# Optimization experiments

Hardware: AMD Instinct MI355X
Metric: run time of the kernel (lower is better)

The kernel has to match this reference:

```python
import jax, jax.numpy as jnp
import numpy as np

E = 8          # num_experts
TOP_K = 2
CAP_RATIO = 1.2


def setup_inputs() -> dict:
    key = jax.random.key(0)
    k1, k2, k3, k4 = jax.random.split(key, 4)
    B, L, D, H = 2, 2048, 768, 2048
    x = jax.random.normal(k1, (B, L, D), dtype=jnp.float32)
    Wg = jax.random.normal(k2, (D, E), dtype=jnp.float32) * 0.02   # gate: Linear(D, E, bias=False)
    W1 = jax.random.normal(k3, (E, D, 2 * H), dtype=jnp.float32) * 0.02  # fc1 per expert (y | gate halves)
    W2 = jax.random.normal(k4, (E, H, D), dtype=jnp.float32) * 0.02      # fc2 per expert
    return {"x": x, "Wg": Wg, "W1": W1, "W2": W2}


def reference(x, Wg, W1, W2):
    B, L, D = x.shape
    H = W2.shape[1]
    xf = x.reshape(-1, D)                      # [N, D]
    N = xf.shape[0]
    capacity = int(CAP_RATIO * N / E)          # static, matches torch int()

    logits = xf @ Wg                           # [N, E]
    scores, idx = jax.lax.top_k(logits, TOP_K) # [N, K] (descending, like torch.topk)
    weights = jax.nn.softmax(scores, axis=-1)  # [N, K]

    # padded token table: row N is a zero token used for unfilled capacity slots
    xpad = jnp.concatenate([xf, jnp.zeros((1, D), xf.dtype)], axis=0)
    wpad_zero = jnp.zeros((1,), weights.dtype)
    out = jnp.zeros((N, D), x.dtype)

    for k in range(TOP_K):
        ik = idx[:, k]                                         # [N] expert id per token
        onehot = (ik[:, None] == jnp.arange(E)[None, :])       # [N, E]
        pos = jnp.cumsum(onehot, axis=0) - 1                   # rank within expert, ascending token order
        posk = jnp.take_along_axis(pos, ik[:, None], axis=1)[:, 0]  # [N]
        keep = posk < capacity                                 # first-come capacity (== indices[:capacity])

        # dispatch buffer [E, C]: token index per slot, N (pad) where unfilled/dropped
        buf = jnp.full((E, capacity), N, dtype=jnp.int32)
        buf = buf.at[ik, posk].set(jnp.arange(N, dtype=jnp.int32), mode="drop")

        xg = xpad[buf]                                         # [E, C, D]
        h = jnp.einsum("ecd,edh->ech", xg, W1)                 # [E, C, 2H]
        act = h[..., :H] * jax.nn.silu(h[..., H:])             # GatedMLP: y * silu(gate)
        ye = jnp.einsum("ech,ehd->ecd", act, W2)               # [E, C, D]

        wk = jnp.where(keep, weights[:, k], 0.0)               # [N]
        w_buf = jnp.concatenate([wk, wpad_zero])[buf]          # [E, C], 0 on pad slots
        out = out.at[buf.reshape(-1)].add(
            (w_buf[..., None] * ye).reshape(E * capacity, D), mode="drop"
        )

    return out.reshape(B, L, D)
```

## Files before the change

### kernel.cpp

```cpp
#include <hip/hip_runtime.h>


typedef _Float16 half8 __attribute__((ext_vector_type(8)));
typedef _Float16 half4t __attribute__((ext_vector_type(4)));
typedef float f4 __attribute__((ext_vector_type(4)));

#define N_TOK 4096
#define DDIM  768
#define HDIM  2048
#define NEXP  8
#define CAP   614
#define CAPP  640

#define XH_OFF    0L
#define W1T_OFF   6292992L
#define W2T_OFF   56624640L
#define ACT_OFF   81790464L
#define EIDX_OFF  123733504L
#define WTS_OFF   123766272L
#define TOKL_OFF  123799040L
#define CNT_OFF   123840000L

__device__ __forceinline__ void gld16(const void* g, void* l) {
  __builtin_amdgcn_global_load_lds(
      (const __attribute__((address_space(1))) unsigned int*)g,
      (__attribute__((address_space(3))) unsigned int*)l, 16, 0, 0);
}

__global__ __launch_bounds__(256) void cvt_tr_kernel(const float* __restrict__ src,
                                                     _Float16* __restrict__ dst,
                                                     int R, int C) {
  __shared__ float tile[64 * 69];
  int e = blockIdx.z;
  int r0 = blockIdx.x * 64, c0 = blockIdx.y * 64;
  long sb = (long)e * R * C;
  int t = threadIdx.x;
  int rrow = t >> 4, c4 = (t & 15) * 4;
#pragma unroll
  for (int i = 0; i < 4; i++) {
    int row = i * 16 + rrow;
    f4 v = *(const f4*)(src + sb + (long)(r0 + row) * C + c0 + c4);
    *(f4*)(&tile[row * 69 + c4]) = v;
  }
  __syncthreads();
#pragma unroll
  for (int s = 0; s < 2; s++) {
    int idx = t + s * 256;
    int c = idx >> 3, ch = idx & 7;
    half8 h;
#pragma unroll
    for (int j = 0; j < 8; j++) h[j] = (_Float16)tile[(ch * 8 + j) * 69 + c];
    *(half8*)(dst + sb + (long)(c0 + c) * R + r0 + ch * 8) = h;
  }
}

__global__ __launch_bounds__(256) void router_kernel(const float* __restrict__ x,
                                                     const float* __restrict__ Wg,
                                                     _Float16* __restrict__ xh,
                                                     int* __restrict__ eidx,
                                                     float* __restrict__ wts) {
  __shared__ float wgT[NEXP * DDIM];
  int t = threadIdx.x;
  for (int i = t; i < DDIM * NEXP; i += 256) wgT[(i & 7) * DDIM + (i >> 3)] = Wg[i];
  __syncthreads();
  int w = t >> 6, lane = t & 63;
  int tok = blockIdx.x * 4 + w;
  if (tok > N_TOK) return;
  if (tok == N_TOK) {
    half4t zz; zz[0] = zz[1] = zz[2] = zz[3] = (_Float16)0.f;
#pragma unroll
    for (int j = 0; j < 3; j++) *(half4t*)(xh + (long)N_TOK * DDIM + (lane + j * 64) * 4) = zz;
    return;
  }
  const float* xr = x + (long)tok * DDIM;
#pragma unroll
  for (int j = 0; j < 3; j++) {
    f4 v = *(const f4*)(xr + (lane + j * 64) * 4);
    half4t hv;
    hv[0] = (_Float16)v[0]; hv[1] = (_Float16)v[1];
    hv[2] = (_Float16)v[2]; hv[3] = (_Float16)v[3];
    *(half4t*)(xh + (long)tok * DDIM + (lane + j * 64) * 4) = hv;
  }
  float acc[8] = {0.f, 0.f, 0.f, 0.f, 0.f, 0.f, 0.f, 0.f};
#pragma unroll
  for (int i = 0; i < 12; i++) {
    float xv = xr[i * 64 + lane];
#pragma unroll
    for (int e2 = 0; e2 < 8; e2++) acc[e2] += xv * wgT[e2 * DDIM + i * 64 + lane];
  }
#pragma unroll
  for (int e2 = 0; e2 < 8; e2++) {
    float v = acc[e2];
    v += __shfl_xor(v, 32); v += __shfl_xor(v, 16); v += __shfl_xor(v, 8);
    v += __shfl_xor(v, 4);  v += __shfl_xor(v, 2);  v += __shfl_xor(v, 1);
    acc[e2] = v;
  }
  if (lane == 0) {
    float m0 = -1e30f; int i0 = 0;
#pragma unroll
    for (int e2 = 0; e2 < 8; e2++) if (acc[e2] > m0) { m0 = acc[e2]; i0 = e2; }
    float m1 = -1e30f; int i1 = 0;
#pragma unroll
    for (int e2 = 0; e2 < 8; e2++) if (e2 != i0 && acc[e2] > m1) { m1 = acc[e2]; i1 = e2; }
    float tt = __expf(m1 - m0);
    float w0 = 1.f / (1.f + tt);
    eidx[tok * 2 + 0] = i0; eidx[tok * 2 + 1] = i1;
    wts[tok * 2 + 0] = w0;  wts[tok * 2 + 1] = 1.f - w0;
  }
}

__global__ __launch_bounds__(64) void scan_kernel(const int* __restrict__ eidx,
                                                  int* __restrict__ toklist,
                                                  int* __restrict__ counts) {
  int z = blockIdx.x;
  int k = z >> 3, e = z & 7;
  int lane = threadIdx.x;
  int mye[64];
#pragma unroll
  for (int c = 0; c < 64; c++) mye[c] = eidx[(c * 64 + lane) * 2 + k];
  int base = 0;
#pragma unroll 4
  for (int c = 0; c < 64; c++) {
    int n = c * 64 + lane;
    bool pred = (mye[c] == e);
    unsigned long long mask = __ballot(pred);
    if (pred) {
      int pos = base + __popcll(mask & ((1ull << lane) - 1ull));
      if (pos < CAP) toklist[z * CAPP + pos] = n;
    }
    base += __popcll(mask);
  }
  if (lane == 0) counts[z] = (base < CAP) ? base : CAP;
}

__global__ __launch_bounds__(512, 2) void gemm1_kernel(const _Float16* __restrict__ xh,
                                                       const _Float16* __restrict__ w1t,
                                                       const int* __restrict__ toklist,
                                                       const int* __restrict__ counts,
                                                       _Float16* __restrict__ act) {
  int i = blockIdx.x;
  int e = i & 7, j = i >> 3;
  int m = j % 3, nk = j / 3;
  int k = nk & 1, n = nk >> 1;
  int z = k * 8 + e;
  int count = counts[z];
  int m0 = m * 256;
  if (m0 >= count) return;
  int n0 = n * 128;

  __shared__ _Float16 lds[2][32768];

  int t = threadIdx.x;
  int u = t & 7, rg = t >> 3;
  int swz = (u ^ (rg & 7)) * 8;

  int tokr[4];
#pragma unroll
  for (int s = 0; s < 4; s++) {
    int r = m0 + s * 64 + rg;
    tokr[s] = (r < count) ? toklist[z * CAPP + r] : N_TOK;
  }

  const _Float16* ag[4];
  const _Float16* bg[4];
  int adst[4], bdst[4];
#pragma unroll
  for (int s = 0; s < 4; s++) {
    int row = s * 64 + rg;
    ag[s] = xh + (long)tokr[s] * DDIM + swz;
    adst[s] = row * 64 + u * 8;
    int rb = row;
    int hc = n0 + ((rb >> 6) << 5) + (rb & 31) + ((rb >> 5) & 1) * 2048;
    bg[s] = w1t + ((long)e * 4096 + hc) * DDIM + swz;
    bdst[s] = 16384 + rb * 64 + u * 8;
  }

  int lane = t & 63, wid = t >> 6;
  int wm = wid >> 2, wn = wid & 3;
  int q = lane >> 4, m16 = lane & 15;

  f4 zero4 = {0.f, 0.f, 0.f, 0.f};
  f4 acc[8][4];
#pragma unroll
  for (int mt = 0; mt < 8; mt++)
#pragma unroll
    for (int ct = 0; ct < 4; ct++) acc[mt][ct] = zero4;

  asm volatile("s_waitcnt vmcnt(0)" ::: "memory");
  __builtin_amdgcn_sched_barrier(0);

#pragma unroll
  for (int s = 0; s < 4; s++) gld16(ag[s], &lds[0][adst[s]]);
#pragma unroll
  for (int s = 0; s < 4; s++) gld16(bg[s], &lds[0][bdst[s]]);
#pragma unroll
  for (int s = 0; s < 4; s++) gld16(ag[s] + 64, &lds[1][adst[s]]);
#pragma unroll
  for (int s = 0; s < 4; s++) gld16(bg[s] + 64, &lds[1][bdst[s]]);
#pragma unroll
  for (int s = 0; s < 4; s++) { ag[s] += 128; bg[s] += 128; }

  for (int t2 = 0; t2 < 12; t2++) {
    int p = t2 & 1;
    const _Float16* A = &lds[p][0];
    const _Float16* B = &lds[p][16384];
    if (t2 < 11) { asm volatile("s_waitcnt vmcnt(8)" ::: "memory"); }
    else         { asm volatile("s_waitcnt vmcnt(0)" ::: "memory"); }
    __builtin_amdgcn_sched_barrier(0);
    __builtin_amdgcn_s_barrier();
    __builtin_amdgcn_sched_barrier(0);

#pragma unroll
    for (int kk = 0; kk < 2; kk++) {
      half8 bfr[4];
#pragma unroll
      for (int ct = 0; ct < 4; ct++) {
        int rb = wn * 64 + ct * 16 + m16;
        bfr[ct] = *(const half8*)(B + rb * 64 + (((kk * 4 + q) ^ (rb & 7)) * 8));
      }
      __builtin_amdgcn_s_setprio(1);
#pragma unroll
      for (int mt = 0; mt < 8; mt++) {
        int row = wm * 128 + mt * 16 + m16;
        half8 a = *(const half8*)(A + row * 64 + (((kk * 4 + q) ^ (row & 7)) * 8));
#pragma unroll
        for (int ct = 0; ct < 4; ct++)
          acc[mt][ct] = __builtin_amdgcn_mfma_f32_16x16x32_f16(a, bfr[ct], acc[mt][ct], 0, 0, 0);
      }
      __builtin_amdgcn_s_setprio(0);
    }
    asm volatile("s_waitcnt lgkmcnt(0)" ::: "memory");
    __builtin_amdgcn_sched_barrier(0);
    __builtin_amdgcn_s_barrier();
    __builtin_amdgcn_sched_barrier(0);
    if (t2 < 10) {
#pragma unroll
      for (int s = 0; s < 4; s++) gld16(ag[s], &lds[p][adst[s]]);
#pragma unroll
      for (int s = 0; s < 4; s++) gld16(bg[s], &lds[p][bdst[s]]);
#pragma unroll
      for (int s = 0; s < 4; s++) { ag[s] += 64; bg[s] += 64; }
    }
    __builtin_amdgcn_sched_barrier(0);
  }

  long ab = (long)z * CAPP * HDIM;
#pragma unroll
  for (int mt = 0; mt < 8; mt++) {
    int row0 = m0 + wm * 128 + mt * 16 + q * 4;
#pragma unroll
    for (int cp = 0; cp < 2; cp++) {
      int col = n0 + wn * 32 + cp * 16 + m16;
#pragma unroll
      for (int r = 0; r < 4; r++) {
        int row = row0 + r;
        if (row < CAPP) {
          float h1 = acc[mt][cp][r], h2 = acc[mt][2 + cp][r];
          float s = h2 / (1.f + __expf(-h2));
          act[ab + (long)row * HDIM + col] = (_Float16)(h1 * s);
        }
      }
    }
  }
}

__global__ __launch_bounds__(512, 2) void gemm2_kernel(const _Float16* __restrict__ act,
                                                       const _Float16* __restrict__ w2t,
                                                       const int* __restrict__ toklist,
                                                       const int* __restrict__ counts,
                                                       const float* __restrict__ wts,
                                                       float* __restrict__ out) {
  int i = blockIdx.x;
  int e = i & 7, j = i >> 3;
  int m = j % 5, nk = j / 5;
  int k = nk & 1, n = nk >> 1;
  int z = k * 8 + e;
  int count = counts[z];
  int m0 = m * 128;
  if (m0 >= count) return;
  int n0 = n * 256;

  __shared__ _Float16 lds[2][24576];
  __shared__ int toksL[128];
  __shared__ float wrow[128];

  int t = threadIdx.x;
  if (t < 128) {
    int r = m0 + t;
    if (r < count) {
      int tok = toklist[z * CAPP + r];
      toksL[t] = tok;
      wrow[t] = wts[tok * 2 + k];
    } else {
      toksL[t] = -1;
      wrow[t] = 0.f;
    }
  }
  __syncthreads();

  int u = t & 7, rg = t >> 3;
  int swz = (u ^ (rg & 7)) * 8;

  const _Float16* ag[2];
  const _Float16* bg[4];
  int adst[2], bdst[4];
#pragma unroll
  for (int s = 0; s < 2; s++) {
    int row = s * 64 + rg;
    ag[s] = act + ((long)z * CAPP + m0 + row) * HDIM + swz;
    adst[s] = row * 64 + u * 8;
  }
#pragma unroll
  for (int s = 0; s < 4; s++) {
    int rb = s * 64 + rg;
    bg[s] = w2t + ((long)e * DDIM + n0 + rb) * HDIM + swz;
    bdst[s] = 8192 + rb * 64 + u * 8;
  }

  int lane = t & 63, wid = t >> 6;
  int wm = wid >> 2, wn = wid & 3;
  int q = lane >> 4, m16 = lane & 15;

  f4 zero4 = {0.f, 0.f, 0.f, 0.f};
  f4 acc[4][4];
#pragma unroll
  for (int mt = 0; mt < 4; mt++)
#pragma unroll
    for (int ct = 0; ct < 4; ct++) acc[mt][ct] = zero4;

#pragma unroll
  for (int s = 0; s < 2; s++) gld16(ag[s], &lds[0][adst[s]]);
#pragma unroll
  for (int s = 0; s < 4; s++) gld16(bg[s], &lds[0][bdst[s]]);
#pragma unroll
  for (int s = 0; s < 2; s++) gld16(ag[s] + 64, &lds[1][adst[s]]);
#pragma unroll
  for (int s = 0; s < 4; s++) gld16(bg[s] + 64, &lds[1][bdst[s]]);
#pragma unroll
  for (int s = 0; s < 2; s++) ag[s] += 128;
#pragma unroll
  for (int s = 0; s < 4; s++) bg[s] += 128;

  for (int t2 = 0; t2 < 32; t2++) {
    int p = t2 & 1;
    const _Float16* A = &lds[p][0];
    const _Float16* B = &lds[p][8192];
    if (t2 < 31) { asm volatile("s_waitcnt vmcnt(6)" ::: "memory"); }
    else         { asm volatile("s_waitcnt vmcnt(0)" ::: "memory"); }
    __builtin_amdgcn_sched_barrier(0);
    __builtin_amdgcn_s_barrier();
    __builtin_amdgcn_sched_barrier(0);

#pragma unroll
    for (int kk = 0; kk < 2; kk++) {
      half8 bfr[4];
#pragma unroll
      for (int ct = 0; ct < 4; ct++) {
        int rb = wn * 64 + ct * 16 + m16;
        bfr[ct] = *(const half8*)(B + rb * 64 + (((kk * 4 + q) ^ (rb & 7)) * 8));
      }
      __builtin_amdgcn_s_setprio(1);
#pragma unroll
      for (int mt = 0; mt < 4; mt++) {
        int row = wm * 64 + mt * 16 + m16;
        half8 a = *(const half8*)(A + row * 64 + (((kk * 4 + q) ^ (row & 7)) * 8));
#pragma unroll
        for (int ct = 0; ct < 4; ct++)
          acc[mt][ct] = __builtin_amdgcn_mfma_f32_16x16x32_f16(a, bfr[ct], acc[mt][ct], 0, 0, 0);
      }
      __builtin_amdgcn_s_setprio(0);
    }
    asm volatile("s_waitcnt lgkmcnt(0)" ::: "memory");
    __builtin_amdgcn_sched_barrier(0);
    __builtin_amdgcn_s_barrier();
    __builtin_amdgcn_sched_barrier(0);
    if (t2 < 30) {
#pragma unroll
      for (int s = 0; s < 2; s++) gld16(ag[s], &lds[p][adst[s]]);
#pragma unroll
      for (int s = 0; s < 4; s++) gld16(bg[s], &lds[p][bdst[s]]);
#pragma unroll
      for (int s = 0; s < 2; s++) ag[s] += 64;
#pragma unroll
      for (int s = 0; s < 4; s++) bg[s] += 64;
    }
    __builtin_amdgcn_sched_barrier(0);
  }

#pragma unroll
  for (int mt = 0; mt < 4; mt++)
#pragma unroll
    for (int ct = 0; ct < 4; ct++)
#pragma unroll
      for (int r = 0; r < 4; r++) {
        int lr = wm * 64 + mt * 16 + q * 4 + r;
        int tok = toksL[lr];
        if (tok >= 0) {
          int col = n0 + wn * 64 + ct * 16 + m16;
          atomicAdd(&out[(long)tok * DDIM + col], wrow[lr] * acc[mt][ct][r]);
        }
      }
}


extern "C" void kernel_launch(void* const* d_in, const int* in_sizes, int n_in,
                              void* d_out, int out_size, void* d_ws, size_t ws_size,
                              hipStream_t stream) {
  const float* x  = (const float*)d_in[0];
  const float* Wg = (const float*)d_in[1];
  const float* W1 = (const float*)d_in[2];
  const float* W2 = (const float*)d_in[3];
  float* out = (float*)d_out;
  char* ws = (char*)d_ws;

  _Float16* xh   = (_Float16*)(ws + XH_OFF);
  _Float16* w1t  = (_Float16*)(ws + W1T_OFF);
  _Float16* w2t  = (_Float16*)(ws + W2T_OFF);
  _Float16* actb = (_Float16*)(ws + ACT_OFF);
  int* eidx      = (int*)(ws + EIDX_OFF);
  float* wts     = (float*)(ws + WTS_OFF);
  int* toklist   = (int*)(ws + TOKL_OFF);
  int* counts    = (int*)(ws + CNT_OFF);

  hipMemsetAsync(d_out, 0, (size_t)out_size * sizeof(float), stream);
  cvt_tr_kernel<<<dim3(12, 64, 8), 256, 0, stream>>>(W1, w1t, 768, 4096);
  cvt_tr_kernel<<<dim3(32, 12, 8), 256, 0, stream>>>(W2, w2t, 2048, 768);
  router_kernel<<<1025, 256, 0, stream>>>(x, Wg, xh, eidx, wts);
  scan_kernel<<<16, 64, 0, stream>>>(eidx, toklist, counts);
  gemm1_kernel<<<768, 512, 0, stream>>>(xh, w1t, toklist, counts, actb);
  gemm2_kernel<<<240, 512, 0, stream>>>(actb, w2t, toklist, counts, wts, out);
}
```

Measured before the change: 369.3 us.

## Triple-buffer LDS in both expert GEMMs and shrink gemm1 M tile to 128

Both grouped GEMM kernels move from a double-buffered to a three-stage rotating LDS ring. Each K-step is split into two half-steps, and the global-to-LDS loads for the stage two ahead are spread across those halves to overlap memory latency with MFMA work. gemm1 also drops its M tile from 256 to 128 rows, raising its grid from 768 to 1280 blocks and halving accumulator registers. In exchange there are more barriers per iteration, more LDS per block (144 KB), and more B-tile reloads for gemm1. The row<CAPP guard in the gemm1 epilogue is removed, which is safe with 128-row tiles because the last tile ends exactly at 640.

```diff
diff --git a/kernel.cpp b/kernel.cpp
--- a/kernel.cpp
+++ b/kernel.cpp
@@ -20,6 +20,8 @@
 #define WTS_OFF   123766272L
 #define TOKL_OFF  123799040L
 #define CNT_OFF   123840000L
+
+#define BUFH 24576
 
 __device__ __forceinline__ void gld16(const void* g, void* l) {
   __builtin_amdgcn_global_load_lds(
@@ -140,39 +142,41 @@
                                                        _Float16* __restrict__ act) {
   int i = blockIdx.x;
   int e = i & 7, j = i >> 3;
-  int m = j % 3, nk = j / 3;
+  int m = j % 5, nk = j / 5;
   int k = nk & 1, n = nk >> 1;
   int z = k * 8 + e;
   int count = counts[z];
-  int m0 = m * 256;
+  int m0 = m * 128;
   if (m0 >= count) return;
   int n0 = n * 128;
 
-  __shared__ _Float16 lds[2][32768];
+  __shared__ _Float16 lds[3 * BUFH];
 
   int t = threadIdx.x;
   int u = t & 7, rg = t >> 3;
   int swz = (u ^ (rg & 7)) * 8;
 
-  int tokr[4];
-#pragma unroll
-  for (int s = 0; s < 4; s++) {
+  int tokr[2];
+#pragma unroll
+  for (int s = 0; s < 2; s++) {
     int r = m0 + s * 64 + rg;
     tokr[s] = (r < count) ? toklist[z * CAPP + r] : N_TOK;
   }
 
-  const _Float16* ag[4];
-  const _Float16* bg[4];
-  int adst[4], bdst[4];
-#pragma unroll
-  for (int s = 0; s < 4; s++) {
+  const _Float16* ag[2]; int adst[2];
+#pragma unroll
+  for (int s = 0; s < 2; s++) {
     int row = s * 64 + rg;
     ag[s] = xh + (long)tokr[s] * DDIM + swz;
     adst[s] = row * 64 + u * 8;
-    int rb = row;
+  }
+  const _Float16* bg[4]; int bdst[4];
+#pragma unroll
+  for (int s = 0; s < 4; s++) {
+    int rb = s * 64 + rg;
     int hc = n0 + ((rb >> 6) << 5) + (rb & 31) + ((rb >> 5) & 1) * 2048;
     bg[s] = w1t + ((long)e * 4096 + hc) * DDIM + swz;
-    bdst[s] = 16384 + rb * 64 + u * 8;
+    bdst[s] = 8192 + rb * 64 + u * 8;
   }
 
   int lane = t & 63, wid = t >> 6;
@@ -180,9 +184,9 @@
   int q = lane >> 4, m16 = lane & 15;
 
   f4 zero4 = {0.f, 0.f, 0.f, 0.f};
-  f4 acc[8][4];
-#pragma unroll
-  for (int mt = 0; mt < 8; mt++)
+  f4 acc[4][4];
+#pragma unroll
+  for (int mt = 0; mt < 4; mt++)
 #pragma unroll
     for (int ct = 0; ct < 4; ct++) acc[mt][ct] = zero4;
 
@@ -190,75 +194,119 @@
   __builtin_amdgcn_sched_barrier(0);
 
 #pragma unroll
-  for (int s = 0; s < 4; s++) gld16(ag[s], &lds[0][adst[s]]);
-#pragma unroll
-  for (int s = 0; s < 4; s++) gld16(bg[s], &lds[0][bdst[s]]);
-#pragma unroll
-  for (int s = 0; s < 4; s++) gld16(ag[s] + 64, &lds[1][adst[s]]);
-#pragma unroll
-  for (int s = 0; s < 4; s++) gld16(bg[s] + 64, &lds[1][bdst[s]]);
-#pragma unroll
-  for (int s = 0; s < 4; s++) { ag[s] += 128; bg[s] += 128; }
+  for (int s = 0; s < 2; s++) gld16(ag[s], &lds[adst[s]]);
+#pragma unroll
+  for (int s = 0; s < 4; s++) gld16(bg[s], &lds[bdst[s]]);
+#pragma unroll
+  for (int s = 0; s < 2; s++) gld16(ag[s] + 64, &lds[BUFH + adst[s]]);
+#pragma unroll
+  for (int s = 0; s < 4; s++) gld16(bg[s] + 64, &lds[BUFH + bdst[s]]);
+#pragma unroll
+  for (int s = 0; s < 2; s++) ag[s] += 128;
+#pragma unroll
+  for (int s = 0; s < 4; s++) bg[s] += 128;
+  asm volatile("s_waitcnt vmcnt(6)" ::: "memory");
+  __builtin_amdgcn_sched_barrier(0);
+  __builtin_amdgcn_s_barrier();
+  __builtin_amdgcn_sched_barrier(0);
+
+  int offR = 0, offM = BUFH, offW = 2 * BUFH;
 
   for (int t2 = 0; t2 < 12; t2++) {
-    int p = t2 & 1;
-    const _Float16* A = &lds[p][0];
-    const _Float16* B = &lds[p][16384];
-    if (t2 < 11) { asm volatile("s_waitcnt vmcnt(8)" ::: "memory"); }
-    else         { asm volatile("s_waitcnt vmcnt(0)" ::: "memory"); }
+    const _Float16* A = &lds[offR];
+    const _Float16* B = &lds[offR + 8192];
+    bool st = (t2 < 10);
+
+    half8 bfr[4][2], afr[2][2];
+#pragma unroll
+    for (int ct = 0; ct < 4; ct++) {
+      int rb = wn * 64 + ct * 16 + m16;
+      bfr[ct][0] = *(const half8*)(B + rb * 64 + (((0 * 4 + q) ^ (rb & 7)) * 8));
+      bfr[ct][1] = *(const half8*)(B + rb * 64 + (((1 * 4 + q) ^ (rb & 7)) * 8));
+    }
+#pragma unroll
+    for (int mt = 0; mt < 2; mt++) {
+      int row = wm * 64 + mt * 16 + m16;
+      afr[mt][0] = *(const half8*)(A + row * 64 + (((0 * 4 + q) ^ (row & 7)) * 8));
+      afr[mt][1] = *(const half8*)(A + row * 64 + (((1 * 4 + q) ^ (row & 7)) * 8));
+    }
+    if (st) {
+      gld16(ag[0], &lds[offW + adst[0]]);
+      gld16(ag[1], &lds[offW + adst[1]]);
+      gld16(bg[0], &lds[offW + bdst[0]]);
+    }
     __builtin_amdgcn_sched_barrier(0);
     __builtin_amdgcn_s_barrier();
     __builtin_amdgcn_sched_barrier(0);
-
-#pragma unroll
-    for (int kk = 0; kk < 2; kk++) {
-      half8 bfr[4];
+    asm volatile("s_waitcnt lgkmcnt(0)" ::: "memory");
+    __builtin_amdgcn_sched_barrier(0);
+    __builtin_amdgcn_s_setprio(1);
+#pragma unroll
+    for (int mt = 0; mt < 2; mt++)
 #pragma unroll
       for (int ct = 0; ct < 4; ct++) {
-        int rb = wn * 64 + ct * 16 + m16;
-        bfr[ct] = *(const half8*)(B + rb * 64 + (((kk * 4 + q) ^ (rb & 7)) * 8));
+        acc[mt][ct] = __builtin_amdgcn_mfma_f32_16x16x32_f16(afr[mt][0], bfr[ct][0], acc[mt][ct], 0, 0, 0);
+        acc[mt][ct] = __builtin_amdgcn_mfma_f32_16x16x32_f16(afr[mt][1], bfr[ct][1], acc[mt][ct], 0, 0, 0);
       }
-      __builtin_amdgcn_s_setprio(1);
-#pragma unroll
-      for (int mt = 0; mt < 8; mt++) {
-        int row = wm * 128 + mt * 16 + m16;
-        half8 a = *(const half8*)(A + row * 64 + (((kk * 4 + q) ^ (row & 7)) * 8));
-#pragma unroll
-        for (int ct = 0; ct < 4; ct++)
-          acc[mt][ct] = __builtin_amdgcn_mfma_f32_16x16x32_f16(a, bfr[ct], acc[mt][ct], 0, 0, 0);
+    __builtin_amdgcn_s_setprio(0);
+    __builtin_amdgcn_sched_barrier(0);
+    __builtin_amdgcn_s_barrier();
+    __builtin_amdgcn_sched_barrier(0);
+
+    half8 afr2[2][2];
+#pragma unroll
+    for (int mt = 0; mt < 2; mt++) {
+      int row = wm * 64 + (2 + mt) * 16 + m16;
+      afr2[mt][0] = *(const half8*)(A + row * 64 + (((0 * 4 + q) ^ (row & 7)) * 8));
+      afr2[mt][1] = *(const half8*)(A + row * 64 + (((1 * 4 + q) ^ (row & 7)) * 8));
+    }
+    if (st) {
+      gld16(bg[1], &lds[offW + bdst[1]]);
+      gld16(bg[2], &lds[offW + bdst[2]]);
+      gld16(bg[3], &lds[offW + bdst[3]]);
+#pragma unroll
+      for (int s = 0; s < 2; s++) ag[s] += 64;
+#pragma unroll
+      for (int s = 0; s < 4; s++) bg[s] += 64;
+    }
+    __builtin_amdgcn_sched_barrier(0);
+    __builtin_amdgcn_s_barrier();
+    __builtin_amdgcn_sched_barrier(0);
+    asm volatile("s_waitcnt lgkmcnt(0)" ::: "memory");
+    __builtin_amdgcn_sched_barrier(0);
+    __builtin_amdgcn_s_setprio(1);
+#pragma unroll
+    for (int mt = 0; mt < 2; mt++)
+#pragma unroll
+      for (int ct = 0; ct < 4; ct++) {
+        acc[2 + mt][ct] = __builtin_amdgcn_mfma_f32_16x16x32_f16(afr2[mt][0], bfr[ct][0], acc[2 + mt][ct], 0, 0, 0);
+        acc[2 + mt][ct] = __builtin_amdgcn_mfma_f32_16x16x32_f16(afr2[mt][1], bfr[ct][1], acc[2 + mt][ct], 0, 0, 0);
       }
-      __builtin_amdgcn_s_setprio(0);
-    }
-    asm volatile("s_waitcnt lgkmcnt(0)" ::: "memory");
-    __builtin_amdgcn_sched_barrier(0);
-    __builtin_amdgcn_s_barrier();
-    __builtin_amdgcn_sched_barrier(0);
-    if (t2 < 10) {
-#pragma unroll
-      for (int s = 0; s < 4; s++) gld16(ag[s], &lds[p][adst[s]]);
-#pragma unroll
-      for (int s = 0; s < 4; s++) gld16(bg[s], &lds[p][bdst[s]]);
-#pragma unroll
-      for (int s = 0; s < 4; s++) { ag[s] += 64; bg[s] += 64; }
-    }
-    __builtin_amdgcn_sched_barrier(0);
+    __builtin_amdgcn_s_setprio(0);
+    __builtin_amdgcn_sched_barrier(0);
+    if (t2 < 10)      { asm volatile("s_waitcnt vmcnt(6)" ::: "memory"); }
+    else if (t2 == 10){ asm volatile("s_waitcnt vmcnt(0)" ::: "memory"); }
+    if (t2 < 11) {
+      __builtin_amdgcn_sched_barrier(0);
+      __builtin_amdgcn_s_barrier();
+      __builtin_amdgcn_sched_barrier(0);
+    }
+    int tmp = offR; offR = offM; offM = offW; offW = tmp;
   }
 
   long ab = (long)z * CAPP * HDIM;
 #pragma unroll
-  for (int mt = 0; mt < 8; mt++) {
-    int row0 = m0 + wm * 128 + mt * 16 + q * 4;
+  for (int mt = 0; mt < 4; mt++) {
+    int row0 = m0 + wm * 64 + mt * 16 + q * 4;
 #pragma unroll
     for (int cp = 0; cp < 2; cp++) {
       int col = n0 + wn * 32 + cp * 16 + m16;
 #pragma unroll
       for (int r = 0; r < 4; r++) {
         int row = row0 + r;
-        if (row < CAPP) {
-          float h1 = acc[mt][cp][r], h2 = acc[mt][2 + cp][r];
-          float s = h2 / (1.f + __expf(-h2));
-          act[ab + (long)row * HDIM + col] = (_Float16)(h1 * s);
-        }
+        float h1 = acc[mt][cp][r], h2 = acc[mt][2 + cp][r];
+        float s = h2 / (1.f + __expf(-h2));
+        act[ab + (long)row * HDIM + col] = (_Float16)(h1 * s);
       }
     }
   }
@@ -280,7 +328,7 @@
   if (m0 >= count) return;
   int n0 = n * 256;
 
-  __shared__ _Float16 lds[2][24576];
+  __shared__ _Float16 lds[3 * BUFH];
   __shared__ int toksL[128];
   __shared__ float wrow[128];
 
@@ -301,15 +349,14 @@
   int u = t & 7, rg = t >> 3;
   int swz = (u ^ (rg & 7)) * 8;
 
-  const _Float16* ag[2];
-  const _Float16* bg[4];
-  int adst[2], bdst[4];
+  const _Float16* ag[2]; int adst[2];
 #pragma unroll
   for (int s = 0; s < 2; s++) {
     int row = s * 64 + rg;
     ag[s] = act + ((long)z * CAPP + m0 + row) * HDIM + swz;
     adst[s] = row * 64 + u * 8;
   }
+  const _Float16* bg[4]; int bdst[4];
 #pragma unroll
   for (int s = 0; s < 4; s++) {
     int rb = s * 64 + rg;
@@ -329,62 +376,104 @@
     for (int ct = 0; ct < 4; ct++) acc[mt][ct] = zero4;
 
 #pragma unroll
-  for (int s = 0; s < 2; s++) gld16(ag[s], &lds[0][adst[s]]);
-#pragma unroll
-  for (int s = 0; s < 4; s++) gld16(bg[s], &lds[0][bdst[s]]);
-#pragma unroll
-  for (int s = 0; s < 2; s++) gld16(ag[s] + 64, &lds[1][adst[s]]);
-#pragma unroll
-  for (int s = 0; s < 4; s++) gld16(bg[s] + 64, &lds[1][bdst[s]]);
+  for (int s = 0; s < 2; s++) gld16(ag[s], &lds[adst[s]]);
+#pragma unroll
+  for (int s = 0; s < 4; s++) gld16(bg[s], &lds[bdst[s]]);
+#pragma unroll
+  for (int s = 0; s < 2; s++) gld16(ag[s] + 64, &lds[BUFH + adst[s]]);
+#pragma unroll
+  for (int s = 0; s < 4; s++) gld16(bg[s] + 64, &lds[BUFH + bdst[s]]);
 #pragma unroll
   for (int s = 0; s < 2; s++) ag[s] += 128;
 #pragma unroll
   for (int s = 0; s < 4; s++) bg[s] += 128;
+  asm volatile("s_waitcnt vmcnt(6)" ::: "memory");
+  __builtin_amdgcn_sched_barrier(0);
+  __builtin_amdgcn_s_barrier();
+  __builtin_amdgcn_sched_barrier(0);
+
+  int offR = 0, offM = BUFH, offW = 2 * BUFH;
 
   for (int t2 = 0; t2 < 32; t2++) {
-    int p = t2 & 1;
-    const _Float16* A = &lds[p][0];
-    const _Float16* B = &lds[p][8192];
-    if (t2 < 31) { asm volatile("s_waitcnt vmcnt(6)" ::: "memory"); }
-    else         { asm volatile("s_waitcnt vmcnt(0)" ::: "memory"); }
+    const _Float16* A = &lds[offR];
+    const _Float16* B = &lds[offR + 8192];
+    bool st = (t2 < 30);
+
+    half8 bfr[4][2], afr[2][2];
+#pragma unroll
+    for (int ct = 0; ct < 4; ct++) {
+      int rb = wn * 64 + ct * 16 + m16;
+      bfr[ct][0] = *(const half8*)(B + rb * 64 + (((0 * 4 + q) ^ (rb & 7)) * 8));
+      bfr[ct][1] = *(const half8*)(B + rb * 64 + (((1 * 4 + q) ^ (rb & 7)) * 8));
+    }
+#pragma unroll
+    for (int mt = 0; mt < 2; mt++) {
+      int row = wm * 64 + mt * 16 + m16;
+      afr[mt][0] = *(const half8*)(A + row * 64 + (((0 * 4 + q) ^ (row & 7)) * 8));
+      afr[mt][1] = *(const half8*)(A + row * 64 + (((1 * 4 + q) ^ (row & 7)) * 8));
+    }
+    if (st) {
+      gld16(ag[0], &lds[offW + adst[0]]);
+      gld16(ag[1], &lds[offW + adst[1]]);
+      gld16(bg[0], &lds[offW + bdst[0]]);
+    }
     __builtin_amdgcn_sched_barrier(0);
     __builtin_amdgcn_s_barrier();
     __builtin_amdgcn_sched_barrier(0);
-
-#pragma unroll
-    for (int kk = 0; kk < 2; kk++) {
-      half8 bfr[4];
+    asm volatile("s_waitcnt lgkmcnt(0)" ::: "memory");
+    __builtin_amdgcn_sched_barrier(0);
+    __builtin_amdgcn_s_setprio(1);
+#pragma unroll
+    for (int mt = 0; mt < 2; mt++)
 #pragma unroll
       for (int ct = 0; ct < 4; ct++) {
-        int rb = wn * 64 + ct * 16 + m16;
-        bfr[ct] = *(const half8*)(B + rb * 64 + (((kk * 4 + q) ^ (rb & 7)) * 8));
+        acc[mt][ct] = __builtin_amdgcn_mfma_f32_16x16x32_f16(afr[mt][0], bfr[ct][0], acc[mt][ct], 0, 0, 0);
+        acc[mt][ct] = __builtin_amdgcn_mfma_f32_16x16x32_f16(afr[mt][1], bfr[ct][1], acc[mt][ct], 0, 0, 0);
       }
-      __builtin_amdgcn_s_setprio(1);
-#pragma unroll
-      for (int mt = 0; mt < 4; mt++) {
-        int row = wm * 64 + mt * 16 + m16;
-        half8 a = *(const half8*)(A + row * 64 + (((kk * 4 + q) ^ (row & 7)) * 8));
-#pragma unroll
-        for (int ct = 0; ct < 4; ct++)
-          acc[mt][ct] = __builtin_amdgcn_mfma_f32_16x16x32_f16(a, bfr[ct], acc[mt][ct], 0, 0, 0);
+    __builtin_amdgcn_s_setprio(0);
+    __builtin_amdgcn_sched_barrier(0);
+    __builtin_amdgcn_s_barrier();
+    __builtin_amdgcn_sched_barrier(0);
+
+    half8 afr2[2][2];
+#pragma unroll
+    for (int mt = 0; mt < 2; mt++) {
+      int row = wm * 64 + (2 + mt) * 16 + m16;
+      afr2[mt][0] = *(const half8*)(A + row * 64 + (((0 * 4 + q) ^ (row & 7)) * 8));
+      afr2[mt][1] = *(const half8*)(A + row * 64 + (((1 * 4 + q) ^ (row & 7)) * 8));
+    }
+    if (st) {
+      gld16(bg[1], &lds[offW + bdst[1]]);
+      gld16(bg[2], &lds[offW + bdst[2]]);
+      gld16(bg[3], &lds[offW + bdst[3]]);
+#pragma unroll
+      for (int s = 0; s < 2; s++) ag[s] += 64;
+#pragma unroll
+      for (int s = 0; s < 4; s++) bg[s] += 64;
+    }
+    __builtin_amdgcn_sched_barrier(0);
+    __builtin_amdgcn_s_barrier();
+    __builtin_amdgcn_sched_barrier(0);
+    asm volatile("s_waitcnt lgkmcnt(0)" ::: "memory");
+    __builtin_amdgcn_sched_barrier(0);
+    __builtin_amdgcn_s_setprio(1);
+#pragma unroll
+    for (int mt = 0; mt < 2; mt++)
+#pragma unroll
+      for (int ct = 0; ct < 4; ct++) {
+        acc[2 + mt][ct] = __builtin_amdgcn_mfma_f32_16x16x32_f16(afr2[mt][0], bfr[ct][0], acc[2 + mt][ct], 0, 0, 0);
+        acc[2 + mt][ct] = __builtin_amdgcn_mfma_f32_16x16x32_f16(afr2[mt][1], bfr[ct][1], acc[2 + mt][ct], 0, 0, 0);
       }
-      __builtin_amdgcn_s_setprio(0);
-    }
-    asm volatile("s_waitcnt lgkmcnt(0)" ::: "memory");
-    __builtin_amdgcn_sched_barrier(0);
-    __builtin_amdgcn_s_barrier();
-    __builtin_amdgcn_sched_barrier(0);
-    if (t2 < 30) {
-#pragma unroll
-      for (int s = 0; s < 2; s++) gld16(ag[s], &lds[p][adst[s]]);
-#pragma unroll
-      for (int s = 0; s < 4; s++) gld16(bg[s], &lds[p][bdst[s]]);
-#pragma unroll
-      for (int s = 0; s < 2; s++) ag[s] += 64;
-#pragma unroll
-      for (int s = 0; s < 4; s++) bg[s] += 64;
-    }
-    __builtin_amdgcn_sched_barrier(0);
+    __builtin_amdgcn_s_setprio(0);
+    __builtin_amdgcn_sched_barrier(0);
+    if (t2 < 30)      { asm volatile("s_waitcnt vmcnt(6)" ::: "memory"); }
+    else if (t2 == 30){ asm volatile("s_waitcnt vmcnt(0)" ::: "memory"); }
+    if (t2 < 31) {
+      __builtin_amdgcn_sched_barrier(0);
+      __builtin_amdgcn_s_barrier();
+      __builtin_amdgcn_sched_barrier(0);
+    }
+    int tmp = offR; offR = offM; offM = offW; offW = tmp;
   }
 
 #pragma unroll
@@ -427,6 +516,6 @@
   cvt_tr_kernel<<<dim3(32, 12, 8), 256, 0, stream>>>(W2, w2t, 2048, 768);
   router_kernel<<<1025, 256, 0, stream>>>(x, Wg, xh, eidx, wts);
   scan_kernel<<<16, 64, 0, stream>>>(eidx, toklist, counts);
-  gemm1_kernel<<<768, 512, 0, stream>>>(xh, w1t, toklist, counts, actb);
+  gemm1_kernel<<<1280, 512, 0, stream>>>(xh, w1t, toklist, counts, actb);
   gemm2_kernel<<<240, 512, 0, stream>>>(actb, w2t, toklist, counts, wts, out);
 }
```

New measurement: 349.7 us. 1.06x faster.
